# Kernel optimization log

Measured on AMD Instinct MI355X. Metric: run time of the kernel, lower is better.

## Reference

```python
import jax, jax.numpy as jnp
import numpy as np

B, S, D, H = 32, 1024, 512, 8
HD = D // H            # head_dim = 64
M = 3                  # modalities: text, image, audio
DIMS = [768, 1024, 512]
LENS = [512, 256, 1024]


def setup_inputs() -> dict:
    key = jax.random.key(0)
    ks = jax.random.split(key, 16)
    inp = {}
    inp['text'] = jax.random.normal(ks[0], (B, LENS[0], DIMS[0]), dtype=jnp.float32)
    inp['image'] = jax.random.normal(ks[1], (B, LENS[1], DIMS[1]), dtype=jnp.float32)
    inp['audio'] = jax.random.normal(ks[2], (B, LENS[2], DIMS[2]), dtype=jnp.float32)
    # per-modality input projections (stored as (in, out); y = x @ W + b)
    for m, (dim, kk, kb) in enumerate(zip(DIMS, ks[3:6], ks[6:9])):
        inp[f'W{m}'] = jax.random.normal(kk, (dim, D), dtype=jnp.float32) * 0.02
        inp[f'b{m}'] = jax.random.normal(kb, (D,), dtype=jnp.float32) * 0.02
    for name, kk in zip(['q', 'k', 'v', 'o'], ks[9:13]):
        inp[f'W{name}'] = jax.random.normal(kk, (D, D), dtype=jnp.float32) * 0.02
        inp[f'b{name}'] = jax.random.normal(jax.random.fold_in(kk, 1), (D,), dtype=jnp.float32) * 0.02
    inp['temperature'] = jnp.asarray(0.07, dtype=jnp.float32)
    inp['attention_weights'] = jnp.ones((3,), dtype=jnp.float32) / 3.0
    inp['role_weights'] = jnp.asarray([1.0, -0.75, 0.75], dtype=jnp.float32)
    return inp


def _forward(text, image, audio, W0, b0, W1, b1, W2, b2,
             Wq, bq, Wk, bk, Wv, bv, Wo, bo,
             temperature, attention_weights, role_weights):
    t_abs = jnp.abs(temperature)

    def proj_pad(x, W, b):
        p = x @ W + b                                   # (B, s, D)
        pad = S - p.shape[1]
        return jnp.pad(p, ((0, 0), (0, pad), (0, 0)))   # (B, S, D)

    feats = jnp.stack([proj_pad(text, W0, b0),
                       proj_pad(image, W1, b1),
                       proj_pad(audio, W2, b2)], axis=0)  # (M, B, S, D)

    # --- standard attention (softmax over the modality axis) ---
    # torch .view(B,H,1,S,hd) is a raw reshape of (B,S,D) -> replicate exactly
    q = (feats[0] @ Wq + bq).reshape(B, H, S, HD)                    # (B,H,S,hd)
    k = (feats @ Wk + bk[None, None, None]).reshape(M, B, H, S, HD)
    v = (feats @ Wv + bv[None, None, None]).reshape(M, B, H, S, HD)
    k = jnp.transpose(k, (1, 2, 0, 3, 4))                            # (B,H,M,S,hd)
    v = jnp.transpose(v, (1, 2, 0, 3, 4))
    scores = jnp.einsum('bhsd,bhmsd->bhms', q, k) / (np.sqrt(HD) * t_abs)
    attn = jax.nn.softmax(scores, axis=2)                            # softmax over modality axis
    mha = jnp.einsum('bhms,bhmsd->bhsd', attn, v)
    mha = jnp.transpose(mha, (0, 2, 1, 3)).reshape(B, S, D)          # (B,S,D)

    # --- angular attention ---
    fn = feats / jnp.maximum(jnp.linalg.norm(feats, axis=-1, keepdims=True), 1e-12)
    cos = jnp.einsum('ibsd,jbsd->bij', fn, fn) / S                   # mean over seq
    angle = jnp.arccos(jnp.clip(cos, -1 + 1e-7, 1 - 1e-7))
    contrib = role_weights[None, None, :] * jnp.exp(-angle / t_abs)  # (B,M,M), j axis last
    offdiag = 1.0 - jnp.eye(M, dtype=feats.dtype)
    ang_scores = (contrib * offdiag[None]).sum(axis=-1)              # (B,M)
    aw = jax.nn.softmax(ang_scores, axis=-1)
    angular_out = jnp.einsum('bm,mbsd->bsd', aw, feats)

    # --- Cayley-Menger volume attention ---
    P = 1 + min(4, M - 1)
    vols = []
    for i in range(M):
        pts = [feats[i]]
        for j in range(min(4, M - 1)):
            ang = (j + 1) * np.pi / 4.0
            other = (i + j + 1) % M
            pts.append(feats[i] * np.cos(ang) + feats[other] * np.sin(ang))
        G = jnp.stack(pts, axis=1).reshape(B, P, S * D)              # (B,P,S*D)
        gram = jnp.einsum('bpk,bqk->bpq', G, G)
        sq = jnp.einsum('bpk,bpk->bp', G, G)
        distsq = sq[:, :, None] + sq[:, None, :] - 2.0 * gram        # ||p-q||^2 summed over s,d
        vols.append(distsq.mean(axis=(1, 2)))
    volumes = jnp.stack(vols, axis=1)                                # (B,M)
    cw = jax.nn.softmax(volumes / t_abs, axis=-1)
    cayley_out = jnp.einsum('bm,mbsd->bsd', cw, feats)

    # --- fuse branches (dropout is identity at p=0 / eval) ---
    w = jax.nn.softmax(attention_weights, axis=0)
    fused = w[0] * mha + w[1] * angular_out + w[2] * cayley_out
    return fused @ Wo + bo


def reference(text, image, audio, W0, b0, W1, b1, W2, b2,
              Wq, bq, Wk, bk, Wv, bv, Wo, bo,
              temperature, attention_weights, role_weights):
    return _forward(text, image, audio, W0, b0, W1, b1, W2, b2,
                    Wq, bq, Wk, bk, Wv, bv, Wo, bo,
                    temperature, attention_weights, role_weights)
```

## Files before the change

kernel.cpp:

```cpp
#include <hip/hip_runtime.h>
#include <hip/hip_bf16.h>


constexpr int CB = 32;
constexpr int CS = 1024;
constexpr int CD = 512;
constexpr int CBS = CB * CS;
constexpr size_t CBSD = (size_t)CBS * CD;

typedef unsigned short u16;
typedef float f32x4 __attribute__((ext_vector_type(4)));
typedef int i32x4 __attribute__((ext_vector_type(4)));

__device__ __forceinline__ float bf2f(u16 u) {
    return __uint_as_float(((unsigned)u) << 16);
}
__device__ __forceinline__ float bfLO(int w) {
    return __uint_as_float(((unsigned)w) << 16);
}
__device__ __forceinline__ float bfHI(int w) {
    return __uint_as_float((unsigned)w & 0xffff0000u);
}
__device__ __forceinline__ u16 f2bf(float f) {
    unsigned u = __float_as_uint(f);
    return (u16)((u + 0x7FFFu + ((u >> 16) & 1u)) >> 16);
}
__device__ __forceinline__ size_t mapRow(int r, int lg) {
    return ((size_t)(r >> lg) << 10) + (size_t)(r & ((1 << lg) - 1));
}

#define GLOAD_LDS16(g, l) __builtin_amdgcn_global_load_lds( \
    (const __attribute__((address_space(1))) void*)(g), \
    (__attribute__((address_space(3))) void*)(l), 16, 0, 0)

template <int EPI>
__global__ __launch_bounds__(256) void gemm_mfma(
    const u16* __restrict__ A, const u16* __restrict__ Wt,
    const float* __restrict__ bias, void* __restrict__ Cv,
    int K, int lgIn, int lgOut,
    const float* __restrict__ scores, const float* __restrict__ coef,
    u16* __restrict__ fused, int m)
{
    __shared__ u16 As[128 * 32];
    __shared__ u16 Bs[128 * 32];
    __shared__ float attnw[256];
    const int tid = threadIdx.x;
    const int lane = tid & 63;
    const int wid = tid >> 6;
    const int wr = wid >> 1, wc = wid & 1;
    const int row0 = blockIdx.x * 128;
    const int n0 = blockIdx.y * 128;

    const int sr0 = wid * 32 + (lane >> 2);
    const int sr1 = sr0 + 16;
    const int kp = (lane & 3) * 8;
    const u16* aSrc0 = A + mapRow(row0 + sr0, lgIn) * (size_t)K + kp;
    const u16* aSrc1 = A + mapRow(row0 + sr1, lgIn) * (size_t)K + kp;
    const u16* bSrc0 = Wt + (size_t)(n0 + sr0) * K + kp;
    const u16* bSrc1 = Wt + (size_t)(n0 + sr1) * K + kp;
    u16* aDst0 = &As[wid * 1024];
    u16* aDst1 = &As[wid * 1024 + 512];
    u16* bDst0 = &Bs[wid * 1024];
    u16* bDst1 = &Bs[wid * 1024 + 512];

    f32x4 acc[4][4];
#pragma unroll
    for (int mr = 0; mr < 4; ++mr)
#pragma unroll
        for (int nr = 0; nr < 4; ++nr)
            acc[mr][nr] = (f32x4){0.f, 0.f, 0.f, 0.f};

    const int koff = (lane >> 4) * 8;
    const int fr = lane & 15;

    for (int k0 = 0; k0 < K; k0 += 32) {
        GLOAD_LDS16(aSrc0 + k0, aDst0);
        GLOAD_LDS16(aSrc1 + k0, aDst1);
        GLOAD_LDS16(bSrc0 + k0, bDst0);
        GLOAD_LDS16(bSrc1 + k0, bDst1);
        __syncthreads();
        i32x4 af[4], bf[4];
#pragma unroll
        for (int mr = 0; mr < 4; ++mr)
            af[mr] = *(const i32x4*)&As[(wr * 64 + mr * 16 + fr) * 32 + koff];
#pragma unroll
        for (int nr = 0; nr < 4; ++nr)
            bf[nr] = *(const i32x4*)&Bs[(wc * 64 + nr * 16 + fr) * 32 + koff];
#pragma unroll
        for (int mr = 0; mr < 4; ++mr)
#pragma unroll
            for (int nr = 0; nr < 4; ++nr)
                asm volatile("v_mfma_f32_16x16x32_bf16 %0, %1, %2, %0"
                             : "+v"(acc[mr][nr]) : "v"(af[mr]), "v"(bf[nr]));
        __syncthreads();
    }
    asm volatile("s_nop 7\n\ts_nop 7\n\ts_nop 7");

    if constexpr (EPI == 2) {
        int r = tid >> 1, bi = tid & 1;
        size_t orow = mapRow(row0 + r, lgOut);
        size_t sidx = orow * 8 + (n0 >> 6) + bi;
        float inv_scale = coef[0], w0c = coef[1];
        float s0 = scores[sidx] * inv_scale;
        float s1 = scores[(size_t)CBS * 8 + sidx] * inv_scale;
        float s2 = scores[(size_t)2 * CBS * 8 + sidx] * inv_scale;
        float mx = fmaxf(s0, fmaxf(s1, s2));
        float e0 = __expf(s0 - mx), e1 = __expf(s1 - mx), e2 = __expf(s2 - mx);
        float sel = (m == 0) ? e0 : ((m == 1) ? e1 : e2);
        attnw[tid] = w0c * sel / (e0 + e1 + e2);
        __syncthreads();
    }

    float bv[4];
#pragma unroll
    for (int nr = 0; nr < 4; ++nr) bv[nr] = bias[n0 + wc * 64 + nr * 16 + fr];
    const int rloc0 = wr * 64 + (lane >> 4) * 4;
#pragma unroll
    for (int mr = 0; mr < 4; ++mr) {
#pragma unroll
        for (int j = 0; j < 4; ++j) {
            const int rloc = rloc0 + mr * 16 + j;
            size_t orow = mapRow(row0 + rloc, lgOut);
            if constexpr (EPI == 2) {
                int b = (int)(orow >> 10), R = (int)(orow & 1023);
                float aw = attnw[rloc * 2 + wc];
                int spBase = ((R & 127) << 3);
                int dpBase = ((R >> 7) << 6);
#pragma unroll
                for (int nr = 0; nr < 4; ++nr) {
                    int cg = n0 + wc * 64 + nr * 16 + fr;
                    float v = acc[mr][nr][j] + bv[nr];
                    size_t off = ((size_t)(b << 10) + spBase + (cg >> 6)) * CD
                               + dpBase + (cg & 63);
                    fused[off] = f2bf(bf2f(fused[off]) + aw * v);
                }
            } else {
#pragma unroll
                for (int nr = 0; nr < 4; ++nr) {
                    float v = acc[mr][nr][j] + bv[nr];
                    int col = n0 + wc * 64 + nr * 16 + fr;
                    if constexpr (EPI == 0)
                        ((u16*)Cv)[orow * CD + col] = f2bf(v);
                    else
                        ((float*)Cv)[orow * CD + col] = v;
                }
            }
        }
    }
}

__global__ __launch_bounds__(256) void cvt_f32_bf16(
    const float* __restrict__ in, u16* __restrict__ out, int n4)
{
    int i = blockIdx.x * 256 + threadIdx.x;
    if (i < n4) {
        float4 v = ((const float4*)in)[i];
        ((ushort4*)out)[i] = make_ushort4(f2bf(v.x), f2bf(v.y), f2bf(v.z), f2bf(v.w));
    }
}

__global__ void transpose_w(const float* __restrict__ W, u16* __restrict__ Wt, int K)
{
    __shared__ u16 t[32][33];
    int k0 = blockIdx.x * 32, n0 = blockIdx.y * 32;
    int tx = threadIdx.x, ty = threadIdx.y;
#pragma unroll
    for (int i = 0; i < 4; ++i)
        t[ty + i * 8][tx] = f2bf(W[(size_t)(k0 + ty + i * 8) * 512 + n0 + tx]);
    __syncthreads();
#pragma unroll
    for (int i = 0; i < 4; ++i)
        Wt[(size_t)(n0 + ty + i * 8) * K + k0 + tx] = t[tx][ty + i * 8];
}

struct TP5 { const float* src[5]; u16* dst[5]; };
__global__ void transpose5(TP5 tp)
{
    __shared__ u16 t[32][33];
    const float* W = tp.src[blockIdx.z];
    u16* Wt = tp.dst[blockIdx.z];
    int k0 = blockIdx.x * 32, n0 = blockIdx.y * 32;
    int tx = threadIdx.x, ty = threadIdx.y;
#pragma unroll
    for (int i = 0; i < 4; ++i)
        t[ty + i * 8][tx] = f2bf(W[(size_t)(k0 + ty + i * 8) * 512 + n0 + tx]);
    __syncthreads();
#pragma unroll
    for (int i = 0; i < 4; ++i)
        Wt[(size_t)(n0 + ty + i * 8) * 512 + k0 + tx] = t[tx][ty + i * 8];
}

__global__ void fill_rows_bf16(u16* __restrict__ dst, const float* __restrict__ bias,
                               int Lstart)
{
    int s = Lstart + blockIdx.x;
    int b = blockIdx.y;
    ushort4* r = (ushort4*)(dst + ((size_t)b * CS + s) * CD);
    int c = threadIdx.x;
    float4 bv = ((const float4*)bias)[c];
    r[c] = make_ushort4(f2bf(bv.x), f2bf(bv.y), f2bf(bv.z), f2bf(bv.w));
}

__global__ void zero_rows_bf16(u16* __restrict__ dst, int Lstart)
{
    int s = Lstart + blockIdx.x;
    int b = blockIdx.y;
    ushort4* r = (ushort4*)(dst + ((size_t)b * CS + s) * CD);
    r[threadIdx.x] = make_ushort4(0, 0, 0, 0);
}

__global__ __launch_bounds__(256) void scores_kernel(
    const u16* __restrict__ q, const u16* __restrict__ k,
    float* __restrict__ scoresM)
{
    int wave = threadIdx.x >> 6, lane = threadIdx.x & 63;
    int r0 = blockIdx.x * 32 + wave * 8;
    const u16* qb = q + (size_t)r0 * CD + lane * 8;
    const u16* kb = k + (size_t)r0 * CD + lane * 8;
#pragma unroll
    for (int t = 0; t < 8; ++t) {
        i32x4 qu = *(const i32x4*)(qb + t * CD);
        i32x4 ku = *(const i32x4*)(kb + t * CD);
        float p = 0.f;
#pragma unroll
        for (int j = 0; j < 4; ++j) {
            p = fmaf(bfLO(qu[j]), bfLO(ku[j]), p);
            p = fmaf(bfHI(qu[j]), bfHI(ku[j]), p);
        }
        p += __shfl_xor(p, 1, 64);
        p += __shfl_xor(p, 2, 64);
        p += __shfl_xor(p, 4, 64);
        if ((lane & 7) == 0)
            scoresM[(size_t)(r0 + t) * 8 + (lane >> 3)] = p;
    }
}

__global__ __launch_bounds__(256) void stats_kernel(
    const u16* __restrict__ feats, float* __restrict__ accum)
{
    int wave = threadIdx.x >> 6, lane = threadIdx.x & 63;
    int chunk = blockIdx.x * 4 + wave;
    int r0 = chunk * 16;
    int b = r0 >> 10;
    float a0 = 0, a1 = 0, a2 = 0, a3 = 0, a4 = 0, a5 = 0, a6 = 0, a7 = 0, a8 = 0;
    const u16* base = feats + (size_t)r0 * CD + lane * 8;
    for (int t = 0; t < 16; ++t) {
        const u16* f0 = base + (size_t)t * CD;
        i32x4 u0 = *(const i32x4*)f0;
        i32x4 u1 = *(const i32x4*)(f0 + CBSD);
        i32x4 u2 = *(const i32x4*)(f0 + 2 * CBSD);
        float d00 = 0, d11 = 0, d22 = 0, d01 = 0, d02 = 0, d12 = 0;
#pragma unroll
        for (int j = 0; j < 4; ++j) {
            float x0 = bfLO(u0[j]), y0 = bfHI(u0[j]);
            float x1 = bfLO(u1[j]), y1 = bfHI(u1[j]);
            float x2 = bfLO(u2[j]), y2 = bfHI(u2[j]);
            d00 = fmaf(x0, x0, d00); d00 = fmaf(y0, y0, d00);
            d11 = fmaf(x1, x1, d11); d11 = fmaf(y1, y1, d11);
            d22 = fmaf(x2, x2, d22); d22 = fmaf(y2, y2, d22);
            d01 = fmaf(x0, x1, d01); d01 = fmaf(y0, y1, d01);
            d02 = fmaf(x0, x2, d02); d02 = fmaf(y0, y2, d02);
            d12 = fmaf(x1, x2, d12); d12 = fmaf(y1, y2, d12);
        }
#pragma unroll
        for (int off = 32; off >= 1; off >>= 1) {
            d00 += __shfl_xor(d00, off, 64);
            d11 += __shfl_xor(d11, off, 64);
            d22 += __shfl_xor(d22, off, 64);
            d01 += __shfl_xor(d01, off, 64);
            d02 += __shfl_xor(d02, off, 64);
            d12 += __shfl_xor(d12, off, 64);
        }
        float n0 = fmaxf(sqrtf(d00), 1e-12f);
        float n1 = fmaxf(sqrtf(d11), 1e-12f);
        float n2 = fmaxf(sqrtf(d22), 1e-12f);
        a0 += d00; a1 += d11; a2 += d22; a3 += d01; a4 += d02; a5 += d12;
        a6 += d01 / (n0 * n1); a7 += d02 / (n0 * n2); a8 += d12 / (n1 * n2);
    }
    if (lane == 0) {
        float* acc = accum + b * 9;
        atomicAdd(acc + 0, a0); atomicAdd(acc + 1, a1); atomicAdd(acc + 2, a2);
        atomicAdd(acc + 3, a3); atomicAdd(acc + 4, a4); atomicAdd(acc + 5, a5);
        atomicAdd(acc + 6, a6); atomicAdd(acc + 7, a7); atomicAdd(acc + 8, a8);
    }
}

__global__ void finalize_kernel(const float* __restrict__ accum,
                                const float* __restrict__ temp,
                                const float* __restrict__ attw,
                                const float* __restrict__ rolew,
                                float* __restrict__ coef)
{
    float t_abs = fabsf(temp[0]);
    float x0 = attw[0], x1 = attw[1], x2 = attw[2];
    float mx = fmaxf(x0, fmaxf(x1, x2));
    float e0 = expf(x0 - mx), e1 = expf(x1 - mx), e2 = expf(x2 - mx);
    float inv = 1.0f / (e0 + e1 + e2);
    float w0 = e0 * inv, w1 = e1 * inv, w2 = e2 * inv;
    int b = threadIdx.x;
    if (b == 0) { coef[0] = 1.0f / (8.0f * t_abs); coef[1] = w0; }
    if (b < CB) {
        const float* A = accum + b * 9;
        float Fm[3][3];
        Fm[0][0] = A[0]; Fm[1][1] = A[1]; Fm[2][2] = A[2];
        Fm[0][1] = Fm[1][0] = A[3];
        Fm[0][2] = Fm[2][0] = A[4];
        Fm[1][2] = Fm[2][1] = A[5];
        float cn[3] = {A[6], A[7], A[8]};
        float eij[3];
#pragma unroll
        for (int p = 0; p < 3; ++p) {
            float c = cn[p] * (1.0f / 1024.0f);
            c = fminf(fmaxf(c, -1.0f + 1e-7f), 1.0f - 1e-7f);
            eij[p] = expf(-acosf(c) / t_abs);
        }
        float r0 = rolew[0], r1 = rolew[1], r2 = rolew[2];
        float as0 = r1 * eij[0] + r2 * eij[1];
        float as1 = r0 * eij[0] + r2 * eij[2];
        float as2 = r0 * eij[1] + r1 * eij[2];
        float amx = fmaxf(as0, fmaxf(as1, as2));
        float ea0 = expf(as0 - amx), ea1 = expf(as1 - amx), ea2 = expf(as2 - amx);
        float ainv = 1.0f / (ea0 + ea1 + ea2);
        float awv[3] = {ea0 * ainv, ea1 * ainv, ea2 * ainv};
        const float CA = 0.70710678118654752440f;
        const float C2 = 6.123233995736766e-17f;
        float vols[3];
#pragma unroll
        for (int i = 0; i < 3; ++i) {
            int j1 = (i + 1) % 3, j2 = (i + 2) % 3;
            float G00 = Fm[i][i];
            float G11 = CA * CA * (Fm[i][i] + 2.0f * Fm[i][j1] + Fm[j1][j1]);
            float G22 = C2 * C2 * Fm[i][i] + 2.0f * C2 * Fm[i][j2] + Fm[j2][j2];
            float G01 = CA * (Fm[i][i] + Fm[i][j1]);
            float G02 = C2 * Fm[i][i] + Fm[i][j2];
            float G12 = CA * (C2 * (Fm[i][i] + Fm[i][j1]) + Fm[i][j2] + Fm[j1][j2]);
            vols[i] = (4.0f / 9.0f) * ((G00 + G11 + G22) - (G01 + G02 + G12));
        }
        float vmx = fmaxf(vols[0], fmaxf(vols[1], vols[2]));
        float ev0 = expf((vols[0] - vmx) / t_abs);
        float ev1 = expf((vols[1] - vmx) / t_abs);
        float ev2 = expf((vols[2] - vmx) / t_abs);
        float vinv = 1.0f / (ev0 + ev1 + ev2);
        coef[4 + b * 3 + 0] = w1 * awv[0] + w2 * (ev0 * vinv);
        coef[4 + b * 3 + 1] = w1 * awv[1] + w2 * (ev1 * vinv);
        coef[4 + b * 3 + 2] = w1 * awv[2] + w2 * (ev2 * vinv);
    }
}

__global__ __launch_bounds__(256) void blend_init(
    const u16* __restrict__ feats, const float* __restrict__ scores,
    const float* __restrict__ coef, const float* __restrict__ bv,
    u16* __restrict__ fused)
{
    int bR = blockIdx.x;
    int b = bR >> 10, R = bR & 1023;
    float inv_scale = coef[0], w0c = coef[1];
    float g0 = coef[4 + b * 3 + 0];
    float g1 = coef[4 + b * 3 + 1];
    float g2 = coef[4 + b * 3 + 2];
    int h = R >> 7;
    int spBase = (R & 127) << 3;
#pragma unroll
    for (int it = 0; it < 2; ++it) {
        int c = (it << 8) + threadIdx.x;
        int beta = c >> 6, e = c & 63;
        size_t off = ((size_t)(b << 10) + spBase + beta) * CD + (h << 6) + e;
        float val = g0 * bf2f(feats[off]) + g1 * bf2f(feats[off + CBSD])
                  + g2 * bf2f(feats[off + 2 * CBSD]);
        if (R >= 256) {
            size_t sidx = (size_t)bR * 8 + beta;
            float s0 = scores[sidx] * inv_scale;
            float s1 = scores[(size_t)CBS * 8 + sidx] * inv_scale;
            float s2 = scores[(size_t)2 * CBS * 8 + sidx] * inv_scale;
            float mxs = fmaxf(s0, fmaxf(s1, s2));
            float ex0 = __expf(s0 - mxs), ex1 = __expf(s1 - mxs), ex2 = __expf(s2 - mxs);
            float den = ex0 + ex1 + ex2;
            float bvc = bv[c];
            float t = ex1;
            if (R >= 512) t += ex0;
            val += w0c * (t / den) * bvc;
        }
        fused[off] = f2bf(val);
    }
}

extern "C" void kernel_launch(void* const* d_in, const int* in_sizes, int n_in,
                              void* d_out, int out_size, void* d_ws, size_t ws_size,
                              hipStream_t stream)
{
    const float* text  = (const float*)d_in[0];
    const float* image = (const float*)d_in[1];
    const float* audio = (const float*)d_in[2];
    const float* W0 = (const float*)d_in[3];  const float* b0 = (const float*)d_in[4];
    const float* W1 = (const float*)d_in[5];  const float* b1 = (const float*)d_in[6];
    const float* W2 = (const float*)d_in[7];  const float* b2 = (const float*)d_in[8];
    const float* Wq = (const float*)d_in[9];  const float* bq = (const float*)d_in[10];
    const float* Wk = (const float*)d_in[11]; const float* bk = (const float*)d_in[12];
    const float* Wv = (const float*)d_in[13]; const float* bv = (const float*)d_in[14];
    const float* Wo = (const float*)d_in[15]; const float* bo = (const float*)d_in[16];
    const float* temp  = (const float*)d_in[17];
    const float* attw  = (const float*)d_in[18];
    const float* rolew = (const float*)d_in[19];

    u16* feats  = (u16*)d_ws;
    u16* kv     = feats + 3 * CBSD;
    u16* fused  = kv + CBSD;
    float* scores = (float*)(fused + CBSD);
    float* accum  = scores + (size_t)3 * CBS * 8;
    float* coef   = accum + 320;
    u16* wot      = (u16*)(coef + 128);

    u16* q = (u16*)d_out;
    u16* wpool = q + CBSD;
    u16* w0t = wpool;
    u16* w1t = w0t + 512 * 768;
    u16* w2t = w1t + 512 * 1024;
    u16* wqt = w2t + 512 * 512;
    u16* wkt = wqt + 512 * 512;
    u16* wvt = wkt + 512 * 512;

    const dim3 blk(256);
    const dim3 tblk(32, 8);
    const int Lm[3] = {512, 256, 1024};
    const int lg[3] = {9, 8, 10};
    const float* bm[3] = {b0, b1, b2};
    const float* xm[3] = {text, image, audio};
    u16* wmt[3] = {w0t, w1t, w2t};
    const int Km[3] = {768, 1024, 512};

    zero_rows_bf16<<<dim3(512, CB), dim3(128), 0, stream>>>(feats, 512);
    zero_rows_bf16<<<dim3(768, CB), dim3(128), 0, stream>>>(feats + CBSD, 256);
    hipMemsetAsync(accum, 0, 320 * sizeof(float), stream);

    transpose_w<<<dim3(24, 16), tblk, 0, stream>>>(W0, w0t, 768);
    transpose_w<<<dim3(32, 16), tblk, 0, stream>>>(W1, w1t, 1024);
    TP5 tp;
    tp.src[0] = W2; tp.dst[0] = w2t;
    tp.src[1] = Wq; tp.dst[1] = wqt;
    tp.src[2] = Wk; tp.dst[2] = wkt;
    tp.src[3] = Wv; tp.dst[3] = wvt;
    tp.src[4] = Wo; tp.dst[4] = wot;
    transpose5<<<dim3(16, 16, 5), tblk, 0, stream>>>(tp);

    for (int m = 0; m < 3; ++m) {
        int n = CB * Lm[m] * Km[m];
        cvt_f32_bf16<<<dim3(n / 1024), blk, 0, stream>>>(xm[m], kv, n / 4);
        gemm_mfma<0><<<dim3(CB * Lm[m] / 128, 4), blk, 0, stream>>>(
            kv, wmt[m], bm[m], feats + (size_t)m * CBSD, Km[m], 10, lg[m],
            nullptr, nullptr, nullptr, 0);
    }

    gemm_mfma<0><<<dim3(128, 4), blk, 0, stream>>>(
        feats, wqt, bq, q, 512, 9, 9, nullptr, nullptr, nullptr, 0);
    fill_rows_bf16<<<dim3(512, CB), dim3(128), 0, stream>>>(q, bq, 512);

    stats_kernel<<<dim3(512), blk, 0, stream>>>(feats, accum);
    finalize_kernel<<<dim3(1), dim3(64), 0, stream>>>(accum, temp, attw, rolew, coef);

    for (int m = 0; m < 3; ++m) {
        gemm_mfma<0><<<dim3(CB * Lm[m] / 128, 4), blk, 0, stream>>>(
            feats + (size_t)m * CBSD, wkt, bk, kv, 512, lg[m], lg[m],
            nullptr, nullptr, nullptr, 0);
        if (Lm[m] < CS)
            fill_rows_bf16<<<dim3(CS - Lm[m], CB), dim3(128), 0, stream>>>(kv, bk, Lm[m]);
        scores_kernel<<<dim3(CBS / 32), blk, 0, stream>>>(q, kv, scores + (size_t)m * CBS * 8);
    }

    blend_init<<<dim3(CBS), blk, 0, stream>>>(feats, scores, coef, bv, fused);
    for (int m = 0; m < 3; ++m) {
        gemm_mfma<2><<<dim3(CB * Lm[m] / 128, 4), blk, 0, stream>>>(
            feats + (size_t)m * CBSD, wvt, bv, nullptr, 512, lg[m], lg[m],
            scores, coef, fused, m);
    }

    gemm_mfma<1><<<dim3(256, 4), blk, 0, stream>>>(
        fused, wot, bo, (float*)d_out, 512, 10, 10, nullptr, nullptr, nullptr, 0);
}
```

Measured before the change: 632.4 us.

## Fuse Q·K score computation into K-projection GEMM epilogue and skip padded work

Result: faster. 600.8 us (-5.0%).

```diff
diff --git a/kernel.cpp b/kernel.cpp
--- a/kernel.cpp
+++ b/kernel.cpp
@@ -39,7 +39,8 @@
     const float* __restrict__ bias, void* __restrict__ Cv,
     int K, int lgIn, int lgOut,
     const float* __restrict__ scores, const float* __restrict__ coef,
-    u16* __restrict__ fused, int m)
+    u16* __restrict__ fused, int m,
+    const u16* __restrict__ q16, float* __restrict__ scoresOut)
 {
     __shared__ u16 As[128 * 32];
     __shared__ u16 Bs[128 * 32];
@@ -95,6 +96,35 @@
         __syncthreads();
     }
     asm volatile("s_nop 7\n\ts_nop 7\n\ts_nop 7");
+
+    float bv[4];
+#pragma unroll
+    for (int nr = 0; nr < 4; ++nr) bv[nr] = bias[n0 + wc * 64 + nr * 16 + fr];
+    const int rloc0 = wr * 64 + (lane >> 4) * 4;
+
+    if constexpr (EPI == 3) {
+        const int beta = (n0 >> 6) + wc;
+#pragma unroll
+        for (int mr = 0; mr < 4; ++mr) {
+#pragma unroll
+            for (int j = 0; j < 4; ++j) {
+                const int rloc = rloc0 + mr * 16 + j;
+                size_t orow = mapRow(row0 + rloc, lgOut);
+                const u16* qrow = q16 + orow * CD + n0 + wc * 64 + fr;
+                float p = 0.f;
+#pragma unroll
+                for (int nr = 0; nr < 4; ++nr)
+                    p = fmaf(acc[mr][nr][j] + bv[nr], bf2f(qrow[nr * 16]), p);
+                p += __shfl_xor(p, 1, 64);
+                p += __shfl_xor(p, 2, 64);
+                p += __shfl_xor(p, 4, 64);
+                p += __shfl_xor(p, 8, 64);
+                if (fr == 0)
+                    scoresOut[orow * 8 + beta] = p;
+            }
+        }
+        return;
+    }
 
     if constexpr (EPI == 2) {
         int r = tid >> 1, bi = tid & 1;
@@ -111,10 +141,6 @@
         __syncthreads();
     }
 
-    float bv[4];
-#pragma unroll
-    for (int nr = 0; nr < 4; ++nr) bv[nr] = bias[n0 + wc * 64 + nr * 16 + fr];
-    const int rloc0 = wr * 64 + (lane >> 4) * 4;
 #pragma unroll
     for (int mr = 0; mr < 4; ++mr) {
 #pragma unroll
@@ -209,79 +235,134 @@
     r[threadIdx.x] = make_ushort4(0, 0, 0, 0);
 }
 
-__global__ __launch_bounds__(256) void scores_kernel(
-    const u16* __restrict__ q, const u16* __restrict__ k,
-    float* __restrict__ scoresM)
+__global__ __launch_bounds__(256) void pad_scores(
+    const u16* __restrict__ q, const float* __restrict__ bk,
+    float* __restrict__ scores)
 {
     int wave = threadIdx.x >> 6, lane = threadIdx.x & 63;
-    int r0 = blockIdx.x * 32 + wave * 8;
-    const u16* qb = q + (size_t)r0 * CD + lane * 8;
-    const u16* kb = k + (size_t)r0 * CD + lane * 8;
+    int base = blockIdx.x * 32 + wave * 8;
+    float4 k1 = ((const float4*)bk)[lane * 2];
+    float4 k2 = ((const float4*)bk)[lane * 2 + 1];
 #pragma unroll
     for (int t = 0; t < 8; ++t) {
-        i32x4 qu = *(const i32x4*)(qb + t * CD);
-        i32x4 ku = *(const i32x4*)(kb + t * CD);
+        int id = base + t;
+        int m, bR;
+        if (id < 16384) { m = 0; bR = ((id >> 9) << 10) + 512 + (id & 511); }
+        else {
+            unsigned i2 = id - 16384;
+            unsigned b = i2 / 768u;
+            m = 1; bR = (int)((b << 10) + 256 + (i2 - b * 768u));
+        }
+        i32x4 qu = *(const i32x4*)(q + (size_t)bR * CD + lane * 8);
         float p = 0.f;
-#pragma unroll
-        for (int j = 0; j < 4; ++j) {
-            p = fmaf(bfLO(qu[j]), bfLO(ku[j]), p);
-            p = fmaf(bfHI(qu[j]), bfHI(ku[j]), p);
-        }
+        p = fmaf(bfLO(qu[0]), k1.x, p); p = fmaf(bfHI(qu[0]), k1.y, p);
+        p = fmaf(bfLO(qu[1]), k1.z, p); p = fmaf(bfHI(qu[1]), k1.w, p);
+        p = fmaf(bfLO(qu[2]), k2.x, p); p = fmaf(bfHI(qu[2]), k2.y, p);
+        p = fmaf(bfLO(qu[3]), k2.z, p); p = fmaf(bfHI(qu[3]), k2.w, p);
         p += __shfl_xor(p, 1, 64);
         p += __shfl_xor(p, 2, 64);
         p += __shfl_xor(p, 4, 64);
         if ((lane & 7) == 0)
-            scoresM[(size_t)(r0 + t) * 8 + (lane >> 3)] = p;
-    }
-}
+            scores[(size_t)m * CBS * 8 + (size_t)bR * 8 + (lane >> 3)] = p;
+    }
+}
+
+#define WREDUCE6(d00,d11,d22,d01,d02,d12) \
+    _Pragma("unroll") \
+    for (int off = 32; off >= 1; off >>= 1) { \
+        d00 += __shfl_xor(d00, off, 64); d11 += __shfl_xor(d11, off, 64); \
+        d22 += __shfl_xor(d22, off, 64); d01 += __shfl_xor(d01, off, 64); \
+        d02 += __shfl_xor(d02, off, 64); d12 += __shfl_xor(d12, off, 64); }
 
 __global__ __launch_bounds__(256) void stats_kernel(
     const u16* __restrict__ feats, float* __restrict__ accum)
 {
     int wave = threadIdx.x >> 6, lane = threadIdx.x & 63;
     int chunk = blockIdx.x * 4 + wave;
-    int r0 = chunk * 16;
-    int b = r0 >> 10;
-    float a0 = 0, a1 = 0, a2 = 0, a3 = 0, a4 = 0, a5 = 0, a6 = 0, a7 = 0, a8 = 0;
+    int r0 = chunk * 8;
+    int b = r0 >> 10, s = r0 & 1023;
     const u16* base = feats + (size_t)r0 * CD + lane * 8;
-    for (int t = 0; t < 16; ++t) {
-        const u16* f0 = base + (size_t)t * CD;
-        i32x4 u0 = *(const i32x4*)f0;
-        i32x4 u1 = *(const i32x4*)(f0 + CBSD);
-        i32x4 u2 = *(const i32x4*)(f0 + 2 * CBSD);
-        float d00 = 0, d11 = 0, d22 = 0, d01 = 0, d02 = 0, d12 = 0;
-#pragma unroll
-        for (int j = 0; j < 4; ++j) {
-            float x0 = bfLO(u0[j]), y0 = bfHI(u0[j]);
-            float x1 = bfLO(u1[j]), y1 = bfHI(u1[j]);
-            float x2 = bfLO(u2[j]), y2 = bfHI(u2[j]);
-            d00 = fmaf(x0, x0, d00); d00 = fmaf(y0, y0, d00);
-            d11 = fmaf(x1, x1, d11); d11 = fmaf(y1, y1, d11);
-            d22 = fmaf(x2, x2, d22); d22 = fmaf(y2, y2, d22);
-            d01 = fmaf(x0, x1, d01); d01 = fmaf(y0, y1, d01);
-            d02 = fmaf(x0, x2, d02); d02 = fmaf(y0, y2, d02);
-            d12 = fmaf(x1, x2, d12); d12 = fmaf(y1, y2, d12);
-        }
-#pragma unroll
-        for (int off = 32; off >= 1; off >>= 1) {
-            d00 += __shfl_xor(d00, off, 64);
-            d11 += __shfl_xor(d11, off, 64);
-            d22 += __shfl_xor(d22, off, 64);
-            d01 += __shfl_xor(d01, off, 64);
-            d02 += __shfl_xor(d02, off, 64);
-            d12 += __shfl_xor(d12, off, 64);
-        }
-        float n0 = fmaxf(sqrtf(d00), 1e-12f);
-        float n1 = fmaxf(sqrtf(d11), 1e-12f);
-        float n2 = fmaxf(sqrtf(d22), 1e-12f);
-        a0 += d00; a1 += d11; a2 += d22; a3 += d01; a4 += d02; a5 += d12;
-        a6 += d01 / (n0 * n1); a7 += d02 / (n0 * n2); a8 += d12 / (n1 * n2);
-    }
-    if (lane == 0) {
-        float* acc = accum + b * 9;
-        atomicAdd(acc + 0, a0); atomicAdd(acc + 1, a1); atomicAdd(acc + 2, a2);
-        atomicAdd(acc + 3, a3); atomicAdd(acc + 4, a4); atomicAdd(acc + 5, a5);
-        atomicAdd(acc + 6, a6); atomicAdd(acc + 7, a7); atomicAdd(acc + 8, a8);
+    float* acc = accum + b * 9;
+
+    if (s >= 512) {
+        float a2 = 0;
+#pragma unroll
+        for (int t = 0; t < 8; ++t) {
+            i32x4 u2 = *(const i32x4*)(base + (size_t)t * CD + 2 * CBSD);
+            float d22 = 0;
+#pragma unroll
+            for (int j = 0; j < 4; ++j) {
+                float x = bfLO(u2[j]), y = bfHI(u2[j]);
+                d22 = fmaf(x, x, d22); d22 = fmaf(y, y, d22);
+            }
+#pragma unroll
+            for (int off = 32; off >= 1; off >>= 1) d22 += __shfl_xor(d22, off, 64);
+            a2 += d22;
+        }
+        if (lane == 0) atomicAdd(acc + 2, a2);
+    } else if (s >= 256) {
+        float a0 = 0, a2 = 0, a4 = 0, a7 = 0;
+#pragma unroll
+        for (int t = 0; t < 8; ++t) {
+            const u16* f0 = base + (size_t)t * CD;
+            i32x4 u0 = *(const i32x4*)f0;
+            i32x4 u2 = *(const i32x4*)(f0 + 2 * CBSD);
+            float d00 = 0, d22 = 0, d02 = 0;
+#pragma unroll
+            for (int j = 0; j < 4; ++j) {
+                float x0 = bfLO(u0[j]), y0 = bfHI(u0[j]);
+                float x2 = bfLO(u2[j]), y2 = bfHI(u2[j]);
+                d00 = fmaf(x0, x0, d00); d00 = fmaf(y0, y0, d00);
+                d22 = fmaf(x2, x2, d22); d22 = fmaf(y2, y2, d22);
+                d02 = fmaf(x0, x2, d02); d02 = fmaf(y0, y2, d02);
+            }
+#pragma unroll
+            for (int off = 32; off >= 1; off >>= 1) {
+                d00 += __shfl_xor(d00, off, 64);
+                d22 += __shfl_xor(d22, off, 64);
+                d02 += __shfl_xor(d02, off, 64);
+            }
+            float n0 = fmaxf(sqrtf(d00), 1e-12f);
+            float n2 = fmaxf(sqrtf(d22), 1e-12f);
+            a0 += d00; a2 += d22; a4 += d02; a7 += d02 / (n0 * n2);
+        }
+        if (lane == 0) {
+            atomicAdd(acc + 0, a0); atomicAdd(acc + 2, a2);
+            atomicAdd(acc + 4, a4); atomicAdd(acc + 7, a7);
+        }
+    } else {
+        float a0 = 0, a1 = 0, a2 = 0, a3 = 0, a4 = 0, a5 = 0, a6 = 0, a7 = 0, a8 = 0;
+#pragma unroll
+        for (int t = 0; t < 8; ++t) {
+            const u16* f0 = base + (size_t)t * CD;
+            i32x4 u0 = *(const i32x4*)f0;
+            i32x4 u1 = *(const i32x4*)(f0 + CBSD);
+            i32x4 u2 = *(const i32x4*)(f0 + 2 * CBSD);
+            float d00 = 0, d11 = 0, d22 = 0, d01 = 0, d02 = 0, d12 = 0;
+#pragma unroll
+            for (int j = 0; j < 4; ++j) {
+                float x0 = bfLO(u0[j]), y0 = bfHI(u0[j]);
+                float x1 = bfLO(u1[j]), y1 = bfHI(u1[j]);
+                float x2 = bfLO(u2[j]), y2 = bfHI(u2[j]);
+                d00 = fmaf(x0, x0, d00); d00 = fmaf(y0, y0, d00);
+                d11 = fmaf(x1, x1, d11); d11 = fmaf(y1, y1, d11);
+                d22 = fmaf(x2, x2, d22); d22 = fmaf(y2, y2, d22);
+                d01 = fmaf(x0, x1, d01); d01 = fmaf(y0, y1, d01);
+                d02 = fmaf(x0, x2, d02); d02 = fmaf(y0, y2, d02);
+                d12 = fmaf(x1, x2, d12); d12 = fmaf(y1, y2, d12);
+            }
+            WREDUCE6(d00, d11, d22, d01, d02, d12)
+            float n0 = fmaxf(sqrtf(d00), 1e-12f);
+            float n1 = fmaxf(sqrtf(d11), 1e-12f);
+            float n2 = fmaxf(sqrtf(d22), 1e-12f);
+            a0 += d00; a1 += d11; a2 += d22; a3 += d01; a4 += d02; a5 += d12;
+            a6 += d01 / (n0 * n1); a7 += d02 / (n0 * n2); a8 += d12 / (n1 * n2);
+        }
+        if (lane == 0) {
+            atomicAdd(acc + 0, a0); atomicAdd(acc + 1, a1); atomicAdd(acc + 2, a2);
+            atomicAdd(acc + 3, a3); atomicAdd(acc + 4, a4); atomicAdd(acc + 5, a5);
+            atomicAdd(acc + 6, a6); atomicAdd(acc + 7, a7); atomicAdd(acc + 8, a8);
+        }
     }
 }
 
@@ -447,32 +528,31 @@
         cvt_f32_bf16<<<dim3(n / 1024), blk, 0, stream>>>(xm[m], kv, n / 4);
         gemm_mfma<0><<<dim3(CB * Lm[m] / 128, 4), blk, 0, stream>>>(
             kv, wmt[m], bm[m], feats + (size_t)m * CBSD, Km[m], 10, lg[m],
-            nullptr, nullptr, nullptr, 0);
+            nullptr, nullptr, nullptr, 0, nullptr, nullptr);
     }
 
     gemm_mfma<0><<<dim3(128, 4), blk, 0, stream>>>(
-        feats, wqt, bq, q, 512, 9, 9, nullptr, nullptr, nullptr, 0);
+        feats, wqt, bq, q, 512, 9, 9, nullptr, nullptr, nullptr, 0, nullptr, nullptr);
     fill_rows_bf16<<<dim3(512, CB), dim3(128), 0, stream>>>(q, bq, 512);
 
-    stats_kernel<<<dim3(512), blk, 0, stream>>>(feats, accum);
+    stats_kernel<<<dim3(1024), blk, 0, stream>>>(feats, accum);
     finalize_kernel<<<dim3(1), dim3(64), 0, stream>>>(accum, temp, attw, rolew, coef);
 
     for (int m = 0; m < 3; ++m) {
-        gemm_mfma<0><<<dim3(CB * Lm[m] / 128, 4), blk, 0, stream>>>(
-            feats + (size_t)m * CBSD, wkt, bk, kv, 512, lg[m], lg[m],
-            nullptr, nullptr, nullptr, 0);
-        if (Lm[m] < CS)
-            fill_rows_bf16<<<dim3(CS - Lm[m], CB), dim3(128), 0, stream>>>(kv, bk, Lm[m]);
-        scores_kernel<<<dim3(CBS / 32), blk, 0, stream>>>(q, kv, scores + (size_t)m * CBS * 8);
-    }
+        gemm_mfma<3><<<dim3(CB * Lm[m] / 128, 4), blk, 0, stream>>>(
+            feats + (size_t)m * CBSD, wkt, bk, nullptr, 512, lg[m], lg[m],
+            nullptr, nullptr, nullptr, 0, q, scores + (size_t)m * CBS * 8);
+    }
+    pad_scores<<<dim3(1280), blk, 0, stream>>>(q, bk, scores);
 
     blend_init<<<dim3(CBS), blk, 0, stream>>>(feats, scores, coef, bv, fused);
     for (int m = 0; m < 3; ++m) {
         gemm_mfma<2><<<dim3(CB * Lm[m] / 128, 4), blk, 0, stream>>>(
             feats + (size_t)m * CBSD, wvt, bv, nullptr, 512, lg[m], lg[m],
-            scores, coef, fused, m);
+            scores, coef, fused, m, nullptr, nullptr);
     }
 
     gemm_mfma<1><<<dim3(256, 4), blk, 0, stream>>>(
-        fused, wot, bo, (float*)d_out, 512, 10, 10, nullptr, nullptr, nullptr, 0);
-}
+        fused, wot, bo, (float*)d_out, 512, 10, 10,
+        nullptr, nullptr, nullptr, 0, nullptr, nullptr);
+}
```
